# Optimization experiments

Hardware: AMD Instinct MI355X
Metric: run time of the kernel (lower is better)

## Reference

```python
import jax, jax.numpy as jnp
import numpy as np

ALPHA = 1.0
RANK = 4


def _conv2d_same(x, w):
    # x: [B,C,H,W], w: [O,C,kh,kw], stride 1, 'same' padding
    return jax.lax.conv_general_dilated(
        x, w, window_strides=(1, 1), padding='SAME',
        dimension_numbers=('NCHW', 'OIHW', 'NCHW'))


def setup_inputs() -> dict:
    key = jax.random.key(0)
    k1, k2, k3, k4, k5 = jax.random.split(key, 5)
    B, C, H, W = 32, 64, 64, 256
    O, E, r, k = 64, 4, RANK, 3
    x = jax.random.normal(k1, (B, C, H, W), dtype=jnp.float32)
    subject_id = jax.random.randint(k2, (B,), 0, E, dtype=jnp.int64)
    W_conv = jax.random.normal(k3, (O, C, k, k), dtype=jnp.float32) * (1.0 / np.sqrt(C * k * k))
    W_A = jax.random.normal(k4, (E, r, C, k, k), dtype=jnp.float32) * 0.02
    # torch init zeros W_B; use random here so the LoRA path is numerically exercised
    W_B = jax.random.normal(k5, (E, O, r), dtype=jnp.float32) * 0.02
    return {'x': x, 'subject_id': subject_id, 'W_conv': W_conv, 'W_A': W_A, 'W_B': W_B}


def reference(x, subject_id, W_conv, W_A, W_B):
    B, C, H, W = x.shape
    E, r = W_A.shape[0], W_A.shape[1]
    k = W_A.shape[-1]
    # Base conv
    out = _conv2d_same(x, W_conv)  # [B,O,H,W]
    # Run all adapter A-convs in one batched conv (E*r tiny output channels),
    # then per-sample select the adapter matching subject_id (same math as the
    # masked per-adapter dispatch in the original).
    a_all = _conv2d_same(x, W_A.reshape(E * r, C, k, k))  # [B,E*r,H,W]
    a_all = a_all.reshape(B, E, r, H, W)
    idx = subject_id[:, None, None, None, None]
    a_sel = jnp.take_along_axis(a_all, idx, axis=1)[:, 0]  # [B,r,H,W]
    wb_sel = W_B[subject_id]  # [B,O,r] (1x1 conv weight per sample)
    lora = (ALPHA / r) * jnp.einsum('bor,brhw->bohw', wb_sel, a_sel)
    return out + lora
```

## Files before the change

kernel.cpp:

```cpp
#include <hip/hip_runtime.h>
#include <hip/hip_bf16.h>

typedef __attribute__((ext_vector_type(8)))  short bf16x8;
typedef __attribute__((ext_vector_type(16))) float f32x16;

constexpr int Bn = 32, Cn = 64, Hn = 64, Wn = 256, On = 64, En = 4, Rn = 4;
constexpr float SCALE = 1.0f / Rn;

constexpr int ROW_B  = 258 * 128;

constexpr int WTILE  = 64;
constexpr int HSTRIP = 8;
constexpr int SLOT_B = 66 * 128;

constexpr size_t WFRAG_B = 294912;
constexpr size_t XP_B    = (size_t)Bn * Hn * ROW_B;
constexpr size_t ZROW_B  = ROW_B;

#define GLOAD_LDS16(SRC, DST) \
    __builtin_amdgcn_global_load_lds( \
        (const __attribute__((address_space(1))) void*)(SRC), \
        (__attribute__((address_space(3))) void*)(DST), 16, 0, 0)

__global__ __launch_bounds__(256) void merge_k(
    const float* __restrict__ Wc, const float* __restrict__ Wa,
    const float* __restrict__ Wb, __hip_bfloat16* __restrict__ Wfrag)
{
    int t = blockIdx.x * 256 + threadIdx.x;
    int j    = t & 7;
    int lane = (t >> 3) & 63;
    int g    = t >> 9;
    int s    = g % 36;
    int mh   = (g / 36) & 1;
    int e    = g / 72;
    int m = lane & 31, half = lane >> 5;
    int o = mh * 32 + m;
    int tap = s >> 2, cq = s & 3;
    int c = cq * 16 + half * 8 + j;
    float acc = Wc[(o * Cn + c) * 9 + tap];
#pragma unroll
    for (int r = 0; r < Rn; ++r)
        acc += SCALE * Wb[(e * On + o) * Rn + r] * Wa[((e * Rn + r) * Cn + c) * 9 + tap];
    Wfrag[t] = __float2bfloat16(acc);
}

__global__ __launch_bounds__(256) void pack_k(
    const float* __restrict__ x, __hip_bfloat16* __restrict__ xp,
    __hip_bfloat16* __restrict__ zr)
{
    size_t g = (size_t)blockIdx.x * 256 + threadIdx.x;
    if (blockIdx.x < 8192) {
        int l  = (int)(g & 1023);
        int cb = l & 7;
        int p  = l >> 3;
        int bh = (int)(g >> 10);
        const float* xr = x + ((size_t)(bh >> 6) * Cn * Hn + (bh & 63)) * Wn;
        union { __hip_bfloat16 u[8]; bf16x8 v; } u0, u1;
#pragma unroll
        for (int i = 0; i < 8; ++i) {
            int c = cb * 8 + i;
            float2 L = *reinterpret_cast<const float2*>(xr + (size_t)c * Hn * Wn + 2 * p);
            u0.u[i] = __float2bfloat16(L.x);
            u1.u[i] = __float2bfloat16(L.y);
        }
        char* row = (char*)xp + (size_t)bh * ROW_B;
        int s0 = 2 * p + 1, s1 = 2 * p + 2;
        *reinterpret_cast<bf16x8*>(row + s0 * 128 + ((cb ^ (s0 & 7)) * 16)) = u0.v;
        *reinterpret_cast<bf16x8*>(row + s1 * 128 + ((cb ^ (s1 & 7)) * 16)) = u1.v;
    } else if (blockIdx.x < 8192 + 128) {
        int z = (int)(g - (size_t)8192 * 256);
        int cb = z & 7, t = (z >> 3) & 1, bh = z >> 4;
        char* row = (char*)xp + (size_t)bh * ROW_B;
        bf16x8 zz = {};
        *reinterpret_cast<bf16x8*>(row + (t ? 257 : 0) * 128 + cb * 16) = zz;
    } else {
        int t = (int)(g - (size_t)(8192 + 128) * 256);
        if (t < ROW_B / 16) {
            bf16x8 zz = {};
            reinterpret_cast<bf16x8*>(zr)[t] = zz;
        }
    }
}

__global__ __launch_bounds__(256, 2) void conv9_k(
    const __hip_bfloat16* __restrict__ xp, const __hip_bfloat16* __restrict__ zr,
    const int* __restrict__ sid, const __hip_bfloat16* __restrict__ Wfrag,
    float* __restrict__ out)
{
    __shared__ __align__(16) char xs[4 * SLOT_B];

    const int tid = threadIdx.x;
    const int w0  = blockIdx.x * WTILE;
    const int h0  = blockIdx.y * HSTRIP;
    const int b   = blockIdx.z;
    const int e   = sid[b];
    const size_t HW = (size_t)Hn * Wn;

    const int lane = tid & 63, wave = tid >> 6;
    const int mh = wave & 1, nh = wave >> 1;
    const int n = lane & 31, half = lane >> 5;

    bf16x8 wf[36];
    const bf16x8* wg = reinterpret_cast<const bf16x8*>(Wfrag) + (size_t)(e * 2 + mh) * 36 * 64;
#pragma unroll
    for (int s = 0; s < 36; ++s) wf[s] = wg[s * 64 + lane];

    const char* xpb = (const char*)xp + (size_t)b * Hn * ROW_B + (size_t)w0 * 128;
    const char* zrw = (const char*)zr + (size_t)w0 * 128;
    const int lofs = wave * 1024 + lane * 16;

    auto stage = [&](int rx) {
        const int gh = h0 + rx;
        const char* src = ((unsigned)gh < (unsigned)Hn) ? (xpb + (size_t)gh * ROW_B) : zrw;
        char* dst = xs + ((rx + 1) & 3) * SLOT_B + wave * 1024;
        GLOAD_LDS16(src + lofs,        dst);
        GLOAD_LDS16(src + 4096 + lofs, dst + 4096);
        GLOAD_LDS16(src + 4352 + lofs, dst + 4352);
    };

    stage(-1); stage(0); stage(1);
    __syncthreads();

    for (int st = 0; st < HSTRIP; ++st) {
        stage(st + 2);

        f32x16 a0, a1;
#pragma unroll
        for (int i = 0; i < 16; ++i) { a0[i] = 0.0f; a1[i] = 0.0f; }

#pragma unroll
        for (int s2 = 0; s2 < 18; ++s2) {
            {
                const int s = 2 * s2;
                const int tap = s >> 2, cq = s & 3;
                const int dh = tap / 3, dw = tap % 3;
                int ww = nh * 32 + n + dw;
                const char* p = xs + ((st + dh) & 3) * SLOT_B
                              + ww * 128 + (((cq * 2 + half) ^ (ww & 7)) * 16);
                a0 = __builtin_amdgcn_mfma_f32_32x32x16_bf16(
                        wf[s], *reinterpret_cast<const bf16x8*>(p), a0, 0, 0, 0);
            }
            {
                const int s = 2 * s2 + 1;
                const int tap = s >> 2, cq = s & 3;
                const int dh = tap / 3, dw = tap % 3;
                int ww = nh * 32 + n + dw;
                const char* p = xs + ((st + dh) & 3) * SLOT_B
                              + ww * 128 + (((cq * 2 + half) ^ (ww & 7)) * 16);
                a1 = __builtin_amdgcn_mfma_f32_32x32x16_bf16(
                        wf[s], *reinterpret_cast<const bf16x8*>(p), a1, 0, 0, 0);
            }
        }

        {
            const int hrow = h0 + st;
            size_t base = ((size_t)(b * On + mh * 32 + 4 * half) * Hn + hrow) * Wn
                          + w0 + nh * 32 + n;
#pragma unroll
            for (int r = 0; r < 16; ++r) {
                int o_off = (r & 3) + 8 * (r >> 2);
                out[base + (size_t)o_off * HW] = a0[r] + a1[r];
            }
        }

        __syncthreads();
    }
}

constexpr int FB_WTILE  = 32;
constexpr int FB_HSTRIP = 16;
constexpr int FB_SLOT_B = 34 * 128;

__device__ __forceinline__ int fb_swz(int ww, int cb) {
    return ww * 128 + ((cb ^ ((ww >> 2) & 7)) * 16);
}

__global__ __launch_bounds__(128, 2) void conv8_k(
    const float* __restrict__ x, const int* __restrict__ sid,
    const __hip_bfloat16* __restrict__ Wfrag, float* __restrict__ out)
{
    __shared__ __align__(16) char xs[4 * FB_SLOT_B];

    const int tid = threadIdx.x;
    const int w0  = blockIdx.x * FB_WTILE;
    const int h0  = blockIdx.y * FB_HSTRIP;
    const int b   = blockIdx.z;
    const int e   = sid[b];
    const size_t HW = (size_t)Hn * Wn;

    const int lane = tid & 63, mh = tid >> 6;
    const int n = lane & 31, half = lane >> 5;

    bf16x8 wf[36];
    const bf16x8* wg = reinterpret_cast<const bf16x8*>(Wfrag) + (size_t)(e * 2 + mh) * 36 * 64;
#pragma unroll
    for (int s = 0; s < 36; ++s) wf[s] = wg[s * 64 + lane];

    const int pb = tid >> 3, q = tid & 7;
    const float* xbase = x + ((size_t)b * Cn + pb * 4) * HW + w0 + 4 * q;

    const int hside = tid >> 6, hc = tid & 63;
    const int gwh   = hside ? (w0 + FB_WTILE) : (w0 - 1);
    const bool hv   = (unsigned)gwh < (unsigned)Wn;
    const float* hbase = x + ((size_t)b * Cn + hc) * HW + gwh;

    auto stage_load = [&](float4 (&f)[4], float& hx, int rx) {
        const int gh = h0 + rx;
        if ((unsigned)gh < (unsigned)Hn) {
            const float* src = xbase + (size_t)gh * Wn;
#pragma unroll
            for (int r = 0; r < 4; ++r)
                f[r] = *reinterpret_cast<const float4*>(src + r * HW);
            hx = hv ? hbase[(size_t)gh * Wn] : 0.0f;
        } else {
            float4 z4 = make_float4(0.0f, 0.0f, 0.0f, 0.0f);
#pragma unroll
            for (int r = 0; r < 4; ++r) f[r] = z4;
            hx = 0.0f;
        }
    };
    auto stage_store = [&](float4 (&f)[4], float& hx, int rx) {
        const int slot = (rx + 1) & 3;
        char* dbase = xs + slot * FB_SLOT_B;
        const int cb = pb >> 1, sub = (pb & 1) * 8;
#pragma unroll
        for (int j = 0; j < 4; ++j) {
            union { __hip_bfloat16 u[4]; short4 v; } pk;
#pragma unroll
            for (int r = 0; r < 4; ++r) {
                float v = (j == 0) ? f[r].x : (j == 1) ? f[r].y : (j == 2) ? f[r].z : f[r].w;
                pk.u[r] = __float2bfloat16(v);
            }
            int ww = 4 * q + 1 + j;
            *reinterpret_cast<short4*>(dbase + fb_swz(ww, cb) + sub) = pk.v;
        }
        {
            __hip_bfloat16 hb = __float2bfloat16(hx);
            int ww = hside ? (FB_WTILE + 1) : 0;
            *reinterpret_cast<__hip_bfloat16*>(dbase + fb_swz(ww, hc >> 3) + (hc & 7) * 2) = hb;
        }
    };

    auto barrier = [&]() {
        asm volatile("s_waitcnt lgkmcnt(0)" ::: "memory");
        __builtin_amdgcn_s_barrier();
    };

    float4 fA[4], fB[4];
    float  hxA, hxB;

    stage_load(fA, hxA, -1); stage_store(fA, hxA, -1);
    stage_load(fA, hxA, 0);  stage_store(fA, hxA, 0);
    stage_load(fA, hxA, 1);  stage_store(fA, hxA, 1);
    stage_load(fA, hxA, 2);
    barrier();

    for (int st = 0; st < FB_HSTRIP; ++st) {
        const bool do_issue = (st + 3 <= FB_HSTRIP);
        if (do_issue) {
            if (st & 1) stage_load(fA, hxA, st + 3);
            else        stage_load(fB, hxB, st + 3);
        }

        f32x16 a;
#pragma unroll
        for (int i = 0; i < 16; ++i) a[i] = 0.0f;

#pragma unroll
        for (int s = 0; s < 36; ++s) {
            const int tap = s >> 2, cq = s & 3;
            const int dh = tap / 3, dw = tap % 3;
            const int slotbase = ((st + dh) & 3) * FB_SLOT_B;
            int ww = n + dw;
            bf16x8 bf = *reinterpret_cast<const bf16x8*>(xs + slotbase + fb_swz(ww, cq * 2 + half));
            a = __builtin_amdgcn_mfma_f32_32x32x16_bf16(wf[s], bf, a, 0, 0, 0);
        }

        const bool do_store = (st + 2 <= FB_HSTRIP);
        if (do_store) {
            if (st & 1) stage_store(fB, hxB, st + 2);
            else        stage_store(fA, hxA, st + 2);
        }

        {
            const int hrow = h0 + st;
            size_t base = ((size_t)(b * On + mh * 32 + 4 * half) * Hn + hrow) * Wn + w0 + n;
#pragma unroll
            for (int r = 0; r < 16; ++r) {
                int o_off = (r & 3) + 8 * (r >> 2);
                out[base + (size_t)o_off * HW] = a[r];
            }
        }

        barrier();
    }
}

extern "C" void kernel_launch(void* const* d_in, const int* in_sizes, int n_in,
                              void* d_out, int out_size, void* d_ws, size_t ws_size,
                              hipStream_t stream)
{
    const float* x   = (const float*)d_in[0];
    const int*   sid = (const int*)d_in[1];
    const float* Wc  = (const float*)d_in[2];
    const float* Wa  = (const float*)d_in[3];
    const float* Wb  = (const float*)d_in[4];
    float*       out = (float*)d_out;

    __hip_bfloat16* Wfrag = (__hip_bfloat16*)d_ws;

    merge_k<<<En * 2 * 36 * 64 * 8 / 256, 256, 0, stream>>>(Wc, Wa, Wb, Wfrag);

    const size_t NEED = WFRAG_B + XP_B + ZROW_B;
    if (ws_size >= NEED) {
        __hip_bfloat16* xp = (__hip_bfloat16*)((char*)d_ws + WFRAG_B);
        __hip_bfloat16* zw = (__hip_bfloat16*)((char*)d_ws + WFRAG_B + XP_B);
        pack_k<<<8192 + 128 + 9, 256, 0, stream>>>(x, xp, zw);
        dim3 grid(Wn / WTILE, Hn / HSTRIP, Bn);
        conv9_k<<<grid, 256, 0, stream>>>(xp, zw, sid, Wfrag, out);
    } else {
        dim3 grid(Wn / FB_WTILE, Hn / FB_HSTRIP, Bn);
        conv8_k<<<grid, 128, 0, stream>>>(x, sid, Wfrag, out);
    }
}
```

Before: 283.0 us.

## Vectorize pack loads, remap conv block order, relax per-row barrier waits

The pack kernel now reads float4 per channel and writes four swizzled bf16x8 vectors per thread, halving the block count and widening global loads. The conv kernel flattens its grid and remaps block IDs so consecutive blocks spread across XCD-like groups. The per-row __syncthreads is replaced with an explicit waitcnt that leaves the just-issued prefetch outstanding before the barrier, so the next row's load can overlap compute. The partial vmcnt relies on an assumed count of outstanding loads, which risks a race if the compiler emits a different number of memory ops.

Measured after the change: 277.4 us. 1.02x faster.

```diff
diff --git a/kernel.cpp b/kernel.cpp
--- a/kernel.cpp
+++ b/kernel.cpp
@@ -44,37 +44,42 @@
     Wfrag[t] = __float2bfloat16(acc);
 }
 
-__global__ __launch_bounds__(256) void pack_k(
+__global__ __launch_bounds__(256) void pack2_k(
     const float* __restrict__ x, __hip_bfloat16* __restrict__ xp,
     __hip_bfloat16* __restrict__ zr)
 {
-    size_t g = (size_t)blockIdx.x * 256 + threadIdx.x;
-    if (blockIdx.x < 8192) {
-        int l  = (int)(g & 1023);
-        int cb = l & 7;
-        int p  = l >> 3;
-        int bh = (int)(g >> 10);
-        const float* xr = x + ((size_t)(bh >> 6) * Cn * Hn + (bh & 63)) * Wn;
-        union { __hip_bfloat16 u[8]; bf16x8 v; } u0, u1;
-#pragma unroll
-        for (int i = 0; i < 8; ++i) {
-            int c = cb * 8 + i;
-            float2 L = *reinterpret_cast<const float2*>(xr + (size_t)c * Hn * Wn + 2 * p);
-            u0.u[i] = __float2bfloat16(L.x);
-            u1.u[i] = __float2bfloat16(L.y);
-        }
+    const int blk = blockIdx.x;
+    if (blk < 4096) {
+        int l  = ((blk & 1) << 8) | threadIdx.x;
+        int bh = blk >> 1;
+        int wLo = l & 3, cb = (l >> 2) & 7, wHi = l >> 5;
+        int wq = wHi * 4 + wLo;
+        int b = bh >> 6, h = bh & 63;
+        const float* src = x + (((size_t)(b * Cn + cb * 8) * Hn + h) * Wn) + 4 * wq;
+        float4 f[8];
+#pragma unroll
+        for (int i = 0; i < 8; ++i)
+            f[i] = *reinterpret_cast<const float4*>(src + (size_t)i * Hn * Wn);
         char* row = (char*)xp + (size_t)bh * ROW_B;
-        int s0 = 2 * p + 1, s1 = 2 * p + 2;
-        *reinterpret_cast<bf16x8*>(row + s0 * 128 + ((cb ^ (s0 & 7)) * 16)) = u0.v;
-        *reinterpret_cast<bf16x8*>(row + s1 * 128 + ((cb ^ (s1 & 7)) * 16)) = u1.v;
-    } else if (blockIdx.x < 8192 + 128) {
-        int z = (int)(g - (size_t)8192 * 256);
+#pragma unroll
+        for (int j = 0; j < 4; ++j) {
+            union { __hip_bfloat16 u[8]; bf16x8 v; } pk;
+#pragma unroll
+            for (int i = 0; i < 8; ++i) {
+                float v = (j == 0) ? f[i].x : (j == 1) ? f[i].y : (j == 2) ? f[i].z : f[i].w;
+                pk.u[i] = __float2bfloat16(v);
+            }
+            int s = 4 * wq + 1 + j;
+            *reinterpret_cast<bf16x8*>(row + s * 128 + ((cb ^ (s & 7)) * 16)) = pk.v;
+        }
+    } else if (blk < 4096 + 128) {
+        int z = (blk - 4096) * 256 + threadIdx.x;
         int cb = z & 7, t = (z >> 3) & 1, bh = z >> 4;
         char* row = (char*)xp + (size_t)bh * ROW_B;
         bf16x8 zz = {};
         *reinterpret_cast<bf16x8*>(row + (t ? 257 : 0) * 128 + cb * 16) = zz;
     } else {
-        int t = (int)(g - (size_t)(8192 + 128) * 256);
+        int t = (blk - 4096 - 128) * 256 + threadIdx.x;
         if (t < ROW_B / 16) {
             bf16x8 zz = {};
             reinterpret_cast<bf16x8*>(zr)[t] = zz;
@@ -82,17 +87,19 @@
     }
 }
 
-__global__ __launch_bounds__(256, 2) void conv9_k(
+__global__ __launch_bounds__(256, 2) void conv10_k(
     const __hip_bfloat16* __restrict__ xp, const __hip_bfloat16* __restrict__ zr,
     const int* __restrict__ sid, const __hip_bfloat16* __restrict__ Wfrag,
     float* __restrict__ out)
 {
     __shared__ __align__(16) char xs[4 * SLOT_B];
 
+    const int logical = ((blockIdx.x & 7) << 7) | (blockIdx.x >> 3);
+    const int bx = logical & 3, by = (logical >> 2) & 7, b = logical >> 5;
+
     const int tid = threadIdx.x;
-    const int w0  = blockIdx.x * WTILE;
-    const int h0  = blockIdx.y * HSTRIP;
-    const int b   = blockIdx.z;
+    const int w0  = bx * WTILE;
+    const int h0  = by * HSTRIP;
     const int e   = sid[b];
     const size_t HW = (size_t)Hn * Wn;
 
@@ -119,10 +126,12 @@
     };
 
     stage(-1); stage(0); stage(1);
-    __syncthreads();
+    asm volatile("s_waitcnt vmcnt(0) lgkmcnt(0)" ::: "memory");
+    __builtin_amdgcn_s_barrier();
 
     for (int st = 0; st < HSTRIP; ++st) {
         stage(st + 2);
+        asm volatile("" ::: "memory");
 
         f32x16 a0, a1;
 #pragma unroll
@@ -163,7 +172,8 @@
             }
         }
 
-        __syncthreads();
+        asm volatile("s_waitcnt vmcnt(16) lgkmcnt(0)" ::: "memory");
+        __builtin_amdgcn_s_barrier();
     }
 }
 
@@ -315,9 +325,8 @@
     if (ws_size >= NEED) {
         __hip_bfloat16* xp = (__hip_bfloat16*)((char*)d_ws + WFRAG_B);
         __hip_bfloat16* zw = (__hip_bfloat16*)((char*)d_ws + WFRAG_B + XP_B);
-        pack_k<<<8192 + 128 + 9, 256, 0, stream>>>(x, xp, zw);
-        dim3 grid(Wn / WTILE, Hn / HSTRIP, Bn);
-        conv9_k<<<grid, 256, 0, stream>>>(xp, zw, sid, Wfrag, out);
+        pack2_k<<<4096 + 128 + 9, 256, 0, stream>>>(x, xp, zw);
+        conv10_k<<<dim3(1024, 1, 1), 256, 0, stream>>>(xp, zw, sid, Wfrag, out);
     } else {
         dim3 grid(Wn / FB_WTILE, Hn / FB_HSTRIP, Bn);
         conv8_k<<<grid, 128, 0, stream>>>(x, sid, Wfrag, out);
```
